# Kernel tuning notes

Measured on AMD Instinct MI355X. Metric: run time of the kernel, lower is better.

## Reference

```python
import jax, jax.numpy as jnp
import numpy as np

B, NPG, K = 8, 2048, 20   # graphs, nodes per graph, kNN fanout
N = B * NPG
OUT = 16


def _bn(h, g, b, eps=1e-5):
    # BatchNorm1d (training-mode batch stats, biased var), channels last
    ax = tuple(range(h.ndim - 1))
    m = h.mean(ax)
    v = h.var(ax)
    return g * (h - m) * jax.lax.rsqrt(v + eps) + b


def _mlp(h, w, b, g, be):
    # Sequential(Linear, ReLU, BatchNorm1d)
    return _bn(jax.nn.relu(h @ w + b), g, be)


def _knn(f, k):
    # k nearest (squared euclidean), self included like torch_cluster.knn(x, x)
    sq = jnp.sum(f * f, axis=-1)
    d = sq[:, None] - 2.0 * (f @ f.T) + sq[None, :]   # [n, n]
    return jax.lax.top_k(-d, k)[1]                    # [n, k]


def setup_inputs() -> dict:
    key = jax.random.key(0)
    ks = jax.random.split(key, 16)

    def w(i, shape):
        return jax.random.normal(ks[i], shape, jnp.float32) * (1.0 / np.sqrt(shape[0]))

    return {
        "pos": jax.random.normal(ks[0], (N, 3), jnp.float32),
        "x": jax.random.normal(ks[1], (N, 1), jnp.float32),
        "batch": jnp.repeat(jnp.arange(B, dtype=jnp.int32), NPG),  # equal-size graphs
        # conv1 edge MLP: Linear(8,64)+ReLU+BN
        "w1": w(2, (8, 64)), "b1": jnp.zeros((64,), jnp.float32), "g1": jnp.ones((64,), jnp.float32), "be1": jnp.zeros((64,), jnp.float32),
        # conv2 edge MLP: Linear(128,128)+ReLU+BN
        "w2": w(3, (128, 128)), "b2": jnp.zeros((128,), jnp.float32), "g2": jnp.ones((128,), jnp.float32), "be2": jnp.zeros((128,), jnp.float32),
        # fc: Linear(192,256)+ReLU+BN
        "wf": w(4, (192, 256)), "bf": jnp.zeros((256,), jnp.float32), "gf": jnp.ones((256,), jnp.float32), "bef": jnp.zeros((256,), jnp.float32),
        # out head: Linear(256,128)+ReLU+BN, Linear(128,64)+ReLU+BN, Linear(64,OUT)
        "wo1": w(5, (256, 128)), "bo1": jnp.zeros((128,), jnp.float32), "go1": jnp.ones((128,), jnp.float32), "beo1": jnp.zeros((128,), jnp.float32),
        "wo2": w(6, (128, 64)), "bo2": jnp.zeros((64,), jnp.float32), "go2": jnp.ones((64,), jnp.float32), "beo2": jnp.zeros((64,), jnp.float32),
        "wo3": w(7, (64, OUT)), "bo3": jnp.zeros((OUT,), jnp.float32),
    }


def reference(pos, x, batch, w1, b1, g1, be1, w2, b2, g2, be2,
              wf, bf, gf, bef, wo1, bo1, go1, beo1, wo2, bo2, go2, beo2, wo3, bo3):
    # ---- conv1: DynamicEdgeConv over ALL nodes (called without batch) ----
    f0 = jnp.concatenate([pos, x], axis=-1)            # [N, 4]
    idx1 = _knn(f0, K)                                 # [N, K] global kNN
    xi = f0[:, None, :]                                # [N, 1, 4]
    xj = jnp.take(f0, idx1, axis=0)                    # [N, K, 4]
    e1 = jnp.concatenate([jnp.broadcast_to(xi, xj.shape), xj - xi], axis=-1)  # [N,K,8]
    x1 = _mlp(e1, w1, b1, g1, be1).max(axis=1)         # max aggr -> [N, 64]

    # ---- conv2: DynamicEdgeConv with per-graph kNN (equal-size graphs) ----
    x1b = x1.reshape(B, NPG, -1)                       # [B, n, 64]
    idx2 = jax.vmap(lambda f: _knn(f, K))(x1b)         # [B, n, K] local indices
    xj2 = jax.vmap(lambda f, i: f[i])(x1b, idx2)       # [B, n, K, 64]
    xi2 = x1b[:, :, None, :]
    e2 = jnp.concatenate([jnp.broadcast_to(xi2, xj2.shape), xj2 - xi2], axis=-1)
    e2 = e2.reshape(N, K, 128)                         # BN over all edges jointly
    x2 = _mlp(e2, w2, b2, g2, be2).max(axis=1)         # [N, 128]

    # ---- fc + global max pool + head ----
    h = _mlp(jnp.concatenate([x1, x2], axis=-1), wf, bf, gf, bef)  # [N, 256]
    hp = h.reshape(B, NPG, -1).max(axis=1)             # global_max_pool -> [B, 256]
    hp = _mlp(hp, wo1, bo1, go1, beo1)                 # Dropout(0.5) = identity (eval)
    hp = _mlp(hp, wo2, bo2, go2, beo2)
    logits = hp @ wo3 + bo3                            # [B, OUT]
    return jax.nn.log_softmax(logits, axis=1)
```

## Files before the change

### kernel.cpp

```cpp
#include <hip/hip_runtime.h>
#include <math.h>

#define NPTS 16384
#define KNB 20
#define SCAP 512

typedef __attribute__((ext_vector_type(8))) short short8;
typedef __attribute__((ext_vector_type(4))) float f32x4;

static const size_t OFF_F0   = 0;
static const size_t OFF_SSQ0 = OFF_F0   + (size_t)NPTS*4*4;
static const size_t OFF_IDX1 = OFF_SSQ0 + (size_t)NPTS*4;
static const size_t OFF_XMX1 = OFF_IDX1 + (size_t)NPTS*KNB*4;
static const size_t OFF_XMN1 = OFF_XMX1 + (size_t)NPTS*64*4;
static const size_t OFF_SUM1 = OFF_XMN1 + (size_t)NPTS*64*4;
static const size_t OFF_X1   = OFF_SUM1 + 512;
static const size_t OFF_SSQ1 = OFF_X1   + (size_t)NPTS*64*4;
static const size_t OFF_IDX2 = OFF_SSQ1 + (size_t)NPTS*4;
static const size_t OFF_XMX2 = OFF_IDX2 + (size_t)NPTS*KNB*4;
static const size_t OFF_XMN2 = OFF_XMX2 + (size_t)NPTS*128*4;
static const size_t OFF_SUM2 = OFF_XMN2 + (size_t)NPTS*128*4;
static const size_t OFF_X2   = OFF_SUM2 + 1024;
static const size_t OFF_SUMF = OFF_X2   + (size_t)NPTS*128*4;
static const size_t OFF_HPMX = OFF_SUMF + 2048;
static const size_t OFF_HPMN = OFF_HPMX + 8*256*4;

__device__ __forceinline__ float dot4f(float4 a, float4 b) {
  return a.x*b.x + a.y*b.y + a.z*b.z + a.w*b.w;
}

__device__ __forceinline__ float dot64v(const float* a, const float4* b4) {
  float s = 0.f;
  #pragma unroll
  for (int d4 = 0; d4 < 16; ++d4) {
    float4 b = b4[d4];
    s += a[4*d4+0]*b.x + a[4*d4+1]*b.y + a[4*d4+2]*b.z + a[4*d4+3]*b.w;
  }
  return s;
}

__device__ __forceinline__ short f2bf(float x) {
  union { float f; unsigned u; } v; v.f = x;
  unsigned r = (v.u + 0x7FFFu + ((v.u >> 16) & 1u)) >> 16;
  return (short)r;
}

__device__ __forceinline__ void ce(float& a, int& ai, float& b, int& bi) {
  bool sw = b < a;
  float d0 = sw ? b : a;  float d1 = sw ? a : b;
  int   j0 = sw ? bi : ai; int  j1 = sw ? ai : bi;
  a = d0; ai = j0; b = d1; bi = j1;
}

__device__ __forceinline__ void sort16(float (&d)[16], int (&ix)[16]) {
  #pragma unroll
  for (int k = 2; k <= 16; k <<= 1) {
    #pragma unroll
    for (int j = k >> 1; j > 0; j >>= 1) {
      #pragma unroll
      for (int i = 0; i < 16; ++i) {
        int l = i ^ j;
        if (l > i) {
          if ((i & k) == 0) ce(d[i], ix[i], d[l], ix[l]);
          else              ce(d[l], ix[l], d[i], ix[i]);
        }
      }
    }
  }
}

__device__ __forceinline__ void bimerge32(float (&rd)[32], int (&ri)[32]) {
  #pragma unroll
  for (int j = 16; j > 0; j >>= 1) {
    #pragma unroll
    for (int i = 0; i < 32; ++i) {
      int l = i ^ j;
      if (l > i) ce(rd[i], ri[i], rd[l], ri[l]);
    }
  }
}

__device__ __forceinline__ void merge16(float (&rd)[32], int (&ri)[32],
                                        float (&bd)[16], int (&bi)[16]) {
  #pragma unroll
  for (int k = 0; k < 16; ++k) {
    bool sw = bd[15-k] < rd[16+k];
    rd[16+k] = sw ? bd[15-k] : rd[16+k];
    ri[16+k] = sw ? bi[15-k] : ri[16+k];
  }
  bimerge32(rd, ri);
}

__device__ __forceinline__ void mergelane(float (&rd)[32], int (&ri)[32], int mask) {
  float pd[32]; int pi[32];
  #pragma unroll
  for (int s = 0; s < 32; ++s) { pd[s] = __shfl_xor(rd[s], mask); pi[s] = __shfl_xor(ri[s], mask); }
  #pragma unroll
  for (int k = 0; k < 32; ++k) {
    bool sw = pd[31-k] < rd[k];
    rd[k] = sw ? pd[31-k] : rd[k];
    ri[k] = sw ? pi[31-k] : ri[k];
  }
  bimerge32(rd, ri);
}

__device__ __forceinline__ void vce(float& a, float& b) {
  float lo = fminf(a, b);
  b = fmaxf(a, b);
  a = lo;
}

__device__ __forceinline__ void vsort16(float (&d)[16]) {
  #pragma unroll
  for (int k = 2; k <= 16; k <<= 1) {
    #pragma unroll
    for (int j = k >> 1; j > 0; j >>= 1) {
      #pragma unroll
      for (int i = 0; i < 16; ++i) {
        int l = i ^ j;
        if (l > i) {
          if ((i & k) == 0) vce(d[i], d[l]);
          else              vce(d[l], d[i]);
        }
      }
    }
  }
}

__device__ __forceinline__ void vbimerge32(float (&rd)[32]) {
  #pragma unroll
  for (int j = 16; j > 0; j >>= 1) {
    #pragma unroll
    for (int i = 0; i < 32; ++i) {
      int l = i ^ j;
      if (l > i) vce(rd[i], rd[l]);
    }
  }
}

__device__ __forceinline__ void vmerge16(float (&rd)[32], float (&bd)[16]) {
  #pragma unroll
  for (int k = 0; k < 16; ++k) rd[16+k] = fminf(rd[16+k], bd[15-k]);
  vbimerge32(rd);
}

__device__ __forceinline__ void vmergelane(float (&rd)[32], int mask) {
  float pd[32];
  #pragma unroll
  for (int s = 0; s < 32; ++s) pd[s] = __shfl_xor(rd[s], mask);
  #pragma unroll
  for (int k = 0; k < 32; ++k) rd[k] = fminf(rd[k], pd[31-k]);
  vbimerge32(rd);
}

__global__ void k_init(float* sum1, float* sum2, float* sumF, unsigned* hpmx, unsigned* hpmn) {
  int t = blockIdx.x*256 + threadIdx.x;
  if (t < 128) sum1[t] = 0.f;
  if (t < 256) sum2[t] = 0.f;
  if (t < 512) sumF[t] = 0.f;
  if (t < 2048) { hpmx[t] = 0u; hpmn[t] = 0x7f800000u; }
}

__global__ __launch_bounds__(256) void k_f0(const float* __restrict__ pos, const float* __restrict__ x,
                                            float4* __restrict__ f0, float* __restrict__ ssq) {
  int i = blockIdx.x*256 + threadIdx.x;
  if (i >= NPTS) return;
  float4 f;
  f.x = pos[3*i+0]; f.y = pos[3*i+1]; f.z = pos[3*i+2]; f.w = x[i];
  f0[i] = f;
  ssq[i] = dot4f(f, f);
}

__global__ __launch_bounds__(256) void k_knn1(const float4* __restrict__ f0, const float* __restrict__ ssq,
                                              int* __restrict__ idx1) {
  __shared__ float2 surv[8][SCAP];
  __shared__ int scnt[8];
  __shared__ float rowT[8];
  int t = threadIdx.x;
  int r = t >> 5;
  int lane = t & 31;
  int row = blockIdx.x*8 + r;
  if (t < 8) scnt[t] = 0;
  float4 fi = f0[row];
  float sqi = ssq[row];
  {
    float rd[32];
    #pragma unroll
    for (int s = 0; s < 32; ++s) rd[s] = INFINITY;
    #pragma unroll
    for (int b = 0; b < 4; ++b) {
      float bd[16];
      #pragma unroll
      for (int u = 0; u < 16; ++u) {
        int j = b*512 + u*32 + lane;
        float4 c = f0[j];
        bd[u] = (sqi - 2.f*dot4f(fi, c)) + ssq[j];
      }
      vsort16(bd);
      vmerge16(rd, bd);
    }
    vmergelane(rd, 1); vmergelane(rd, 2); vmergelane(rd, 4);
    vmergelane(rd, 8); vmergelane(rd, 16);
    if (lane == 0) rowT[r] = rd[19];
  }
  __syncthreads();
  {
    float4 fr[8]; float sr[8], Tr[8];
    #pragma unroll
    for (int q = 0; q < 8; ++q) {
      fr[q] = f0[blockIdx.x*8 + q];
      sr[q] = ssq[blockIdx.x*8 + q];
      Tr[q] = rowT[q];
    }
    #pragma unroll 4
    for (int k = 0; k < 64; ++k) {
      int j = k*256 + t;
      float4 c = f0[j];
      float cq = ssq[j];
      #pragma unroll
      for (int q = 0; q < 8; ++q) {
        float d = (sr[q] - 2.f*dot4f(fr[q], c)) + cq;
        if (d <= Tr[q]) {
          int slot = atomicAdd(&scnt[q], 1);
          if (slot < SCAP) surv[q][slot] = make_float2(d, __int_as_float(j));
        }
      }
    }
  }
  __syncthreads();
  int n = scnt[r] < SCAP ? scnt[r] : SCAP;
  float rd[32]; int ri[32];
  #pragma unroll
  for (int s = 0; s < 32; ++s) { rd[s] = INFINITY; ri[s] = 0; }
  {
    float bd[16]; int bix[16];
    #pragma unroll
    for (int u = 0; u < 16; ++u) {
      int s = u*32 + lane;
      if (s < n) { float2 v = surv[r][s]; bd[u] = v.x; bix[u] = __float_as_int(v.y); }
      else       { bd[u] = INFINITY; bix[u] = 0; }
    }
    sort16(bd, bix);
    merge16(rd, ri, bd, bix);
  }
  mergelane(rd, ri, 1); mergelane(rd, ri, 2); mergelane(rd, ri, 4);
  mergelane(rd, ri, 8); mergelane(rd, ri, 16);
  if (lane == 0) {
    int4* p = (int4*)&idx1[row*KNB];
    p[0] = make_int4(ri[0],ri[1],ri[2],ri[3]);
    p[1] = make_int4(ri[4],ri[5],ri[6],ri[7]);
    p[2] = make_int4(ri[8],ri[9],ri[10],ri[11]);
    p[3] = make_int4(ri[12],ri[13],ri[14],ri[15]);
    p[4] = make_int4(ri[16],ri[17],ri[18],ri[19]);
  }
}

__global__ __launch_bounds__(256) void k_mlp1(const float4* __restrict__ f0, const int* __restrict__ idx1,
                                              const float* __restrict__ w1, const float* __restrict__ b1,
                                              float* __restrict__ xmx, float* __restrict__ xmn,
                                              float* __restrict__ sums) {
  __shared__ float rs[256], rs2[256];
  int t = threadIdx.x;
  int c = t & 63;
  int w = t >> 6;
  float wc[8];
  #pragma unroll
  for (int d = 0; d < 8; ++d) wc[d] = w1[d*64 + c];
  float bc = b1[c];
  float s = 0.f, s2 = 0.f;
  for (int p = 0; p < 8; ++p) {
    int i = blockIdx.x*32 + p*4 + w;
    float4 fi = f0[i];
    float mx = -INFINITY, mn = INFINITY;
    #pragma unroll
    for (int k = 0; k < KNB; ++k) {
      int j = idx1[i*KNB + k];
      float4 fj = f0[j];
      float h = bc + fi.x*wc[0] + fi.y*wc[1] + fi.z*wc[2] + fi.w*wc[3]
                   + (fj.x-fi.x)*wc[4] + (fj.y-fi.y)*wc[5] + (fj.z-fi.z)*wc[6] + (fj.w-fi.w)*wc[7];
      h = fmaxf(h, 0.f);
      mx = fmaxf(mx, h); mn = fminf(mn, h);
      s += h; s2 += h*h;
    }
    xmx[i*64+c] = mx; xmn[i*64+c] = mn;
  }
  rs[t] = s; rs2[t] = s2;
  __syncthreads();
  if (t < 64) {
    atomicAdd(&sums[c],      rs[t]+rs[t+64]+rs[t+128]+rs[t+192]);
    atomicAdd(&sums[64+c],   rs2[t]+rs2[t+64]+rs2[t+128]+rs2[t+192]);
  }
}

__global__ __launch_bounds__(256) void k_bn1apply(const float* __restrict__ sums, const float* __restrict__ g,
                                                  const float* __restrict__ be, const float* __restrict__ xmx,
                                                  const float* __restrict__ xmn, float* __restrict__ x1) {
  __shared__ float sc_s[64], sh_s[64];
  int t = threadIdx.x;
  if (t < 64) {
    float m = sums[t] * (1.f/327680.f);
    float v = sums[64+t] * (1.f/327680.f) - m*m;
    float sc = g[t] / sqrtf(v + 1e-5f);
    sc_s[t] = sc; sh_s[t] = be[t] - m*sc;
  }
  __syncthreads();
  int c = t & 63;
  int i = blockIdx.x*4 + (t>>6);
  float sc = sc_s[c], sh = sh_s[c];
  float val = (sc >= 0.f) ? xmx[i*64+c] : xmn[i*64+c];
  x1[i*64+c] = sc*val + sh;
}

__global__ __launch_bounds__(256) void k_wprep(const float* __restrict__ w2, short* __restrict__ wtg) {
  int t = blockIdx.x*256 + threadIdx.x;
  int c = t >> 7, k = t & 127;
  wtg[c*128 + k] = f2bf(w2[k*128 + c]);
}

__global__ __launch_bounds__(256) void k_ssq1(const float* __restrict__ x1, float* __restrict__ ssq1) {
  int i = blockIdx.x*256 + threadIdx.x;
  alignas(16) float f[64];
  #pragma unroll
  for (int d4 = 0; d4 < 16; ++d4) ((float4*)f)[d4] = ((const float4*)x1)[i*16 + d4];
  ssq1[i] = dot64v(f, (const float4*)f);
}

__global__ __launch_bounds__(256) void k_knn2(const float* __restrict__ x1, const float* __restrict__ ssq1,
                                              int* __restrict__ idx2) {
  __shared__ __align__(16) float tf[128][68];
  __shared__ float tq[128];
  int t = threadIdx.x;
  int row = blockIdx.x*32 + (t>>3);
  int lane = t & 7;
  int cbase = (row >> 11) << 11;
  alignas(16) float fi[64];
  #pragma unroll
  for (int d4 = 0; d4 < 16; ++d4) ((float4*)fi)[d4] = ((const float4*)x1)[row*16 + d4];
  float sqi = ssq1[row];
  float rd[32]; int ri[32];
  #pragma unroll
  for (int s = 0; s < 32; ++s) { rd[s] = INFINITY; ri[s] = 0; }
  for (int tile = 0; tile < 16; ++tile) {
    int base = cbase + tile*128;
    __syncthreads();
    for (int v = t; v < 128*16; v += 256) {
      int jl = v >> 4, d4 = v & 15;
      *(float4*)&tf[jl][d4*4] = ((const float4*)x1)[(base+jl)*16 + d4];
    }
    if (t < 128) tq[t] = ssq1[base + t];
    __syncthreads();
    float bd[16]; int bix[16];
    #pragma unroll
    for (int u = 0; u < 16; ++u) {
      int jl = u*8 + lane;
      bd[u] = (sqi - 2.f*dot64v(fi, (const float4*)&tf[jl][0])) + tq[jl];
      bix[u] = base + jl;
    }
    sort16(bd, bix);
    merge16(rd, ri, bd, bix);
  }
  mergelane(rd, ri, 1);
  mergelane(rd, ri, 2);
  mergelane(rd, ri, 4);
  if (lane == 0) {
    int4* p = (int4*)&idx2[row*KNB];
    p[0] = make_int4(ri[0],ri[1],ri[2],ri[3]);
    p[1] = make_int4(ri[4],ri[5],ri[6],ri[7]);
    p[2] = make_int4(ri[8],ri[9],ri[10],ri[11]);
    p[3] = make_int4(ri[12],ri[13],ri[14],ri[15]);
    p[4] = make_int4(ri[16],ri[17],ri[18],ri[19]);
  }
}

__global__ __launch_bounds__(256) void k_mlp2(const float* __restrict__ x1, const int* __restrict__ idx2,
                                              const short* __restrict__ wtg, const float* __restrict__ b2,
                                              float* __restrict__ xmx, float* __restrict__ xmn,
                                              float* __restrict__ sums) {
  __shared__ __align__(16) short Elds[4*32*136];
  __shared__ int js[4][KNB];
  int t = threadIdx.x;
  if (t < 4*KNB) js[t/KNB][t%KNB] = idx2[blockIdx.x*4*KNB + t];
  __syncthreads();
  #pragma unroll
  for (int cc = 0; cc < 8; ++cc) {
    int v = t + cc*256;
    int p  = v >> 9;
    int rr = (v >> 4) & 31;
    int kc = v & 15;
    short8 outv = {0,0,0,0,0,0,0,0};
    if (rr < KNB) {
      int i = blockIdx.x*4 + p;
      float4 a0, a1;
      if (kc < 8) {
        a0 = ((const float4*)x1)[i*16 + kc*2];
        a1 = ((const float4*)x1)[i*16 + kc*2 + 1];
      } else {
        int j = js[p][rr];
        int kk = kc - 8;
        float4 j0 = ((const float4*)x1)[j*16 + kk*2];
        float4 j1 = ((const float4*)x1)[j*16 + kk*2 + 1];
        float4 i0 = ((const float4*)x1)[i*16 + kk*2];
        float4 i1 = ((const float4*)x1)[i*16 + kk*2 + 1];
        a0 = make_float4(j0.x-i0.x, j0.y-i0.y, j0.z-i0.z, j0.w-i0.w);
        a1 = make_float4(j1.x-i1.x, j1.y-i1.y, j1.z-i1.z, j1.w-i1.w);
      }
      outv[0]=f2bf(a0.x); outv[1]=f2bf(a0.y); outv[2]=f2bf(a0.z); outv[3]=f2bf(a0.w);
      outv[4]=f2bf(a1.x); outv[5]=f2bf(a1.y); outv[6]=f2bf(a1.z); outv[7]=f2bf(a1.w);
    }
    *(short8*)&Elds[p*4352 + rr*136 + kc*8] = outv;
  }
  __syncthreads();
  int w = t >> 6, l = t & 63;
  int colA = w*32 + (l & 15);
  int colB = colA + 16;
  short8 bf[2][4];
  #pragma unroll
  for (int n = 0; n < 2; ++n)
    #pragma unroll
    for (int kb = 0; kb < 4; ++kb) {
      int col = w*32 + n*16 + (l & 15);
      int k0 = kb*32 + (l >> 4)*8;
      bf[n][kb] = *(const short8*)&wtg[col*128 + k0];
    }
  float bc0 = b2[colA], bc1 = b2[colB];
  float sT0=0.f, qT0=0.f, sT1=0.f, qT1=0.f;
  #pragma unroll
  for (int p = 0; p < 4; ++p) {
    int i = blockIdx.x*4 + p;
    float mx0=-INFINITY, mn0=INFINITY, s0=0.f, q0=0.f;
    float mx1=-INFINITY, mn1=INFINITY, s1=0.f, q1=0.f;
    #pragma unroll
    for (int m = 0; m < 2; ++m) {
      short8 af[4];
      #pragma unroll
      for (int kb = 0; kb < 4; ++kb) {
        int row = m*16 + (l & 15);
        int k0 = kb*32 + (l >> 4)*8;
        af[kb] = *(short8*)&Elds[p*4352 + row*136 + k0];
      }
      f32x4 acc0 = {0.f,0.f,0.f,0.f};
      f32x4 acc1 = {0.f,0.f,0.f,0.f};
      #pragma unroll
      for (int kb = 0; kb < 4; ++kb) {
        acc0 = __builtin_amdgcn_mfma_f32_16x16x32_bf16(af[kb], bf[0][kb], acc0, 0, 0, 0);
        acc1 = __builtin_amdgcn_mfma_f32_16x16x32_bf16(af[kb], bf[1][kb], acc1, 0, 0, 0);
      }
      int rbase = (l >> 4)*4 + m*16;
      #pragma unroll
      for (int reg = 0; reg < 4; ++reg) {
        bool valid = (rbase + reg) < KNB;
        float h0 = fmaxf(acc0[reg] + bc0, 0.f);
        float h1 = fmaxf(acc1[reg] + bc1, 0.f);
        if (valid) {
          mx0 = fmaxf(mx0, h0); mn0 = fminf(mn0, h0); s0 += h0; q0 += h0*h0;
          mx1 = fmaxf(mx1, h1); mn1 = fminf(mn1, h1); s1 += h1; q1 += h1*h1;
        }
      }
    }
    #pragma unroll
    for (int dlt = 16; dlt <= 32; dlt <<= 1) {
      mx0 = fmaxf(mx0, __shfl_xor(mx0, dlt)); mn0 = fminf(mn0, __shfl_xor(mn0, dlt));
      s0 += __shfl_xor(s0, dlt);              q0 += __shfl_xor(q0, dlt);
      mx1 = fmaxf(mx1, __shfl_xor(mx1, dlt)); mn1 = fminf(mn1, __shfl_xor(mn1, dlt));
      s1 += __shfl_xor(s1, dlt);              q1 += __shfl_xor(q1, dlt);
    }
    if (l < 16) {
      xmx[i*128 + colA] = mx0; xmx[i*128 + colB] = mx1;
      xmn[i*128 + colA] = mn0; xmn[i*128 + colB] = mn1;
    }
    sT0 += s0; qT0 += q0; sT1 += s1; qT1 += q1;
  }
  if (l < 16) {
    atomicAdd(&sums[colA], sT0);       atomicAdd(&sums[colB], sT1);
    atomicAdd(&sums[128 + colA], qT0); atomicAdd(&sums[128 + colB], qT1);
  }
}

__global__ __launch_bounds__(256) void k_bn2apply(const float* __restrict__ sums, const float* __restrict__ g,
                                                  const float* __restrict__ be, const float* __restrict__ xmx,
                                                  const float* __restrict__ xmn, float* __restrict__ x2) {
  __shared__ float sc_s[128], sh_s[128];
  int t = threadIdx.x;
  if (t < 128) {
    float m = sums[t] * (1.f/327680.f);
    float v = sums[128+t] * (1.f/327680.f) - m*m;
    float sc = g[t] / sqrtf(v + 1e-5f);
    sc_s[t] = sc; sh_s[t] = be[t] - m*sc;
  }
  __syncthreads();
  int c = t & 127;
  int i = blockIdx.x*2 + (t>>7);
  float sc = sc_s[c], sh = sh_s[c];
  float val = (sc >= 0.f) ? xmx[i*128+c] : xmn[i*128+c];
  x2[i*128+c] = sc*val + sh;
}

__global__ __launch_bounds__(256) void k_gemmF(const float* __restrict__ x1, const float* __restrict__ x2,
                                               const float* __restrict__ wf, const float* __restrict__ bf,
                                               float* __restrict__ sumsF, unsigned* __restrict__ hpmx,
                                               unsigned* __restrict__ hpmn) {
  __shared__ float A_s[64*193];
  __shared__ __align__(16) float B_s[192*64];
  __shared__ float red[1024];
  int t = threadIdx.x;
  int rt = blockIdx.x >> 2;
  int ct = blockIdx.x & 3;
  for (int v = t; v < 64*48; v += 256) {
    int r = v / 48, gg = v - r*48;
    int row = rt*64 + r;
    float4 e = (gg < 16) ? ((const float4*)x1)[row*16 + gg]
                         : ((const float4*)x2)[row*32 + (gg-16)];
    float* p = &A_s[r*193 + gg*4];
    p[0]=e.x; p[1]=e.y; p[2]=e.z; p[3]=e.w;
  }
  for (int v = t; v < 192*16; v += 256) {
    int d = v >> 4, c4 = v & 15;
    *(float4*)&B_s[d*64 + c4*4] = ((const float4*)wf)[d*64 + ct*16 + c4];
  }
  __syncthreads();
  int rg = t & 15, cg = t >> 4;
  float acc[4][4];
  #pragma unroll
  for (int a=0;a<4;a++) { acc[a][0]=0.f; acc[a][1]=0.f; acc[a][2]=0.f; acc[a][3]=0.f; }
  for (int d = 0; d < 192; ++d) {
    float a0 = A_s[(rg*4+0)*193 + d];
    float a1 = A_s[(rg*4+1)*193 + d];
    float a2 = A_s[(rg*4+2)*193 + d];
    float a3 = A_s[(rg*4+3)*193 + d];
    float b0 = B_s[d*64 + cg];
    float b1 = B_s[d*64 + cg + 16];
    float b2 = B_s[d*64 + cg + 32];
    float b3 = B_s[d*64 + cg + 48];
    acc[0][0]+=a0*b0; acc[0][1]+=a0*b1; acc[0][2]+=a0*b2; acc[0][3]+=a0*b3;
    acc[1][0]+=a1*b0; acc[1][1]+=a1*b1; acc[1][2]+=a1*b2; acc[1][3]+=a1*b3;
    acc[2][0]+=a2*b0; acc[2][1]+=a2*b1; acc[2][2]+=a2*b2; acc[2][3]+=a2*b3;
    acc[3][0]+=a3*b0; acc[3][1]+=a3*b1; acc[3][2]+=a3*b2; acc[3][3]+=a3*b3;
  }
  float hv[4][4];
  #pragma unroll
  for (int ss=0; ss<4; ++ss) {
    float bb = bf[ct*64 + cg + ss*16];
    #pragma unroll
    for (int rr=0; rr<4; ++rr) hv[rr][ss] = fmaxf(acc[rr][ss] + bb, 0.f);
  }
  int b = rt >> 5;
  #pragma unroll
  for (int ss=0; ss<4; ++ss) red[rg*64 + cg + ss*16] = hv[0][ss]+hv[1][ss]+hv[2][ss]+hv[3][ss];
  __syncthreads();
  if (t < 64) {
    float v = 0.f;
    #pragma unroll
    for (int r=0;r<16;r++) v += red[r*64 + t];
    atomicAdd(&sumsF[ct*64 + t], v);
  }
  __syncthreads();
  #pragma unroll
  for (int ss=0; ss<4; ++ss) red[rg*64 + cg + ss*16] =
      hv[0][ss]*hv[0][ss]+hv[1][ss]*hv[1][ss]+hv[2][ss]*hv[2][ss]+hv[3][ss]*hv[3][ss];
  __syncthreads();
  if (t < 64) {
    float v = 0.f;
    #pragma unroll
    for (int r=0;r<16;r++) v += red[r*64 + t];
    atomicAdd(&sumsF[256 + ct*64 + t], v);
  }
  __syncthreads();
  #pragma unroll
  for (int ss=0; ss<4; ++ss) red[rg*64 + cg + ss*16] =
      fmaxf(fmaxf(hv[0][ss],hv[1][ss]), fmaxf(hv[2][ss],hv[3][ss]));
  __syncthreads();
  if (t < 64) {
    float v = -INFINITY;
    #pragma unroll
    for (int r=0;r<16;r++) v = fmaxf(v, red[r*64 + t]);
    atomicMax(&hpmx[b*256 + ct*64 + t], __float_as_uint(v));
  }
  __syncthreads();
  #pragma unroll
  for (int ss=0; ss<4; ++ss) red[rg*64 + cg + ss*16] =
      fminf(fminf(hv[0][ss],hv[1][ss]), fminf(hv[2][ss],hv[3][ss]));
  __syncthreads();
  if (t < 64) {
    float v = INFINITY;
    #pragma unroll
    for (int r=0;r<16;r++) v = fminf(v, red[r*64 + t]);
    atomicMin(&hpmn[b*256 + ct*64 + t], __float_as_uint(v));
  }
}

__global__ __launch_bounds__(256) void k_head(const float* __restrict__ sumsF, const float* __restrict__ gf,
                                              const float* __restrict__ bef,
                                              const unsigned* __restrict__ hpmx, const unsigned* __restrict__ hpmn,
                                              const float* __restrict__ wo1, const float* __restrict__ bo1,
                                              const float* __restrict__ go1, const float* __restrict__ beo1,
                                              const float* __restrict__ wo2, const float* __restrict__ bo2,
                                              const float* __restrict__ go2, const float* __restrict__ beo2,
                                              const float* __restrict__ wo3, const float* __restrict__ bo3,
                                              float* __restrict__ out) {
  __shared__ float hp[8][256];
  __shared__ float u1[8][128];
  __shared__ float u2[8][64];
  __shared__ float lg[8][16];
  int t = threadIdx.x;
  {
    float m = sumsF[t] * (1.f/16384.f);
    float v = sumsF[256+t] * (1.f/16384.f) - m*m;
    float sc = gf[t] / sqrtf(v + 1e-5f);
    float sh = bef[t] - m*sc;
    for (int b = 0; b < 8; ++b) {
      unsigned bits = (sc >= 0.f) ? hpmx[b*256+t] : hpmn[b*256+t];
      hp[b][t] = sc*__uint_as_float(bits) + sh;
    }
  }
  __syncthreads();
  for (int p = t; p < 1024; p += 256) {
    int b = p >> 7, c = p & 127;
    float z = bo1[c];
    for (int d = 0; d < 256; ++d) z += hp[b][d]*wo1[d*128+c];
    u1[b][c] = fmaxf(z, 0.f);
  }
  __syncthreads();
  if (t < 128) {
    float m = 0.f;
    for (int b=0;b<8;b++) m += u1[b][t];
    m *= 0.125f;
    float v = 0.f;
    for (int b=0;b<8;b++) { float dd = u1[b][t]-m; v += dd*dd; }
    v *= 0.125f;
    float sc = go1[t]/sqrtf(v+1e-5f), sh = beo1[t]-m*sc;
    for (int b=0;b<8;b++) u1[b][t] = sc*u1[b][t]+sh;
  }
  __syncthreads();
  for (int p = t; p < 512; p += 256) {
    int b = p >> 6, c = p & 63;
    float z = bo2[c];
    for (int d = 0; d < 128; ++d) z += u1[b][d]*wo2[d*64+c];
    u2[b][c] = fmaxf(z, 0.f);
  }
  __syncthreads();
  if (t < 64) {
    float m = 0.f;
    for (int b=0;b<8;b++) m += u2[b][t];
    m *= 0.125f;
    float v = 0.f;
    for (int b=0;b<8;b++) { float dd = u2[b][t]-m; v += dd*dd; }
    v *= 0.125f;
    float sc = go2[t]/sqrtf(v+1e-5f), sh = beo2[t]-m*sc;
    for (int b=0;b<8;b++) u2[b][t] = sc*u2[b][t]+sh;
  }
  __syncthreads();
  if (t < 128) {
    int b = t >> 4, c = t & 15;
    float z = bo3[c];
    for (int d = 0; d < 64; ++d) z += u2[b][d]*wo3[d*16+c];
    lg[b][c] = z;
  }
  __syncthreads();
  if (t < 8) {
    float m = -INFINITY;
    for (int j=0;j<16;j++) m = fmaxf(m, lg[t][j]);
    float s = 0.f;
    for (int j=0;j<16;j++) s += expf(lg[t][j]-m);
    float ls = logf(s);
    for (int j=0;j<16;j++) out[t*16+j] = (lg[t][j]-m) - ls;
  }
}

extern "C" void kernel_launch(void* const* d_in, const int* in_sizes, int n_in,
                              void* d_out, int out_size, void* d_ws, size_t ws_size,
                              hipStream_t stream) {
  (void)in_sizes; (void)n_in; (void)out_size; (void)ws_size;
  const float* pos = (const float*)d_in[0];
  const float* x   = (const float*)d_in[1];
  const float* w1  = (const float*)d_in[3];
  const float* b1  = (const float*)d_in[4];
  const float* g1  = (const float*)d_in[5];
  const float* be1 = (const float*)d_in[6];
  const float* w2  = (const float*)d_in[7];
  const float* b2  = (const float*)d_in[8];
  const float* g2  = (const float*)d_in[9];
  const float* be2 = (const float*)d_in[10];
  const float* wf  = (const float*)d_in[11];
  const float* bf  = (const float*)d_in[12];
  const float* gf  = (const float*)d_in[13];
  const float* bef = (const float*)d_in[14];
  const float* wo1 = (const float*)d_in[15];
  const float* bo1 = (const float*)d_in[16];
  const float* go1 = (const float*)d_in[17];
  const float* beo1= (const float*)d_in[18];
  const float* wo2 = (const float*)d_in[19];
  const float* bo2 = (const float*)d_in[20];
  const float* go2 = (const float*)d_in[21];
  const float* beo2= (const float*)d_in[22];
  const float* wo3 = (const float*)d_in[23];
  const float* bo3 = (const float*)d_in[24];

  char* ws = (char*)d_ws;
  float4*   f0    = (float4*)  (ws + OFF_F0);
  float*    ssq0  = (float*)   (ws + OFF_SSQ0);
  int*      idx1  = (int*)     (ws + OFF_IDX1);
  float*    xmx1  = (float*)   (ws + OFF_XMX1);
  float*    xmn1  = (float*)   (ws + OFF_XMN1);
  float*    sum1  = (float*)   (ws + OFF_SUM1);
  float*    x1    = (float*)   (ws + OFF_X1);
  float*    ssq1  = (float*)   (ws + OFF_SSQ1);
  int*      idx2  = (int*)     (ws + OFF_IDX2);
  float*    xmx2  = (float*)   (ws + OFF_XMX2);
  float*    xmn2  = (float*)   (ws + OFF_XMN2);
  float*    sum2  = (float*)   (ws + OFF_SUM2);
  float*    x2    = (float*)   (ws + OFF_X2);
  float*    sumF  = (float*)   (ws + OFF_SUMF);
  unsigned* hpmx  = (unsigned*)(ws + OFF_HPMX);
  unsigned* hpmn  = (unsigned*)(ws + OFF_HPMN);
  short*    wtg   = (short*)   (ws + OFF_XMX1);

  k_init    <<<8,    256, 0, stream>>>(sum1, sum2, sumF, hpmx, hpmn);
  k_f0      <<<64,   256, 0, stream>>>(pos, x, f0, ssq0);
  k_knn1    <<<2048, 256, 0, stream>>>(f0, ssq0, idx1);
  k_mlp1    <<<512,  256, 0, stream>>>(f0, idx1, w1, b1, xmx1, xmn1, sum1);
  k_bn1apply<<<4096, 256, 0, stream>>>(sum1, g1, be1, xmx1, xmn1, x1);
  k_wprep   <<<64,   256, 0, stream>>>(w2, wtg);
  k_ssq1    <<<64,   256, 0, stream>>>(x1, ssq1);
  k_knn2    <<<512,  256, 0, stream>>>(x1, ssq1, idx2);
  k_mlp2    <<<4096, 256, 0, stream>>>(x1, idx2, wtg, b2, xmx2, xmn2, sum2);
  k_bn2apply<<<8192, 256, 0, stream>>>(sum2, g2, be2, xmx2, xmn2, x2);
  k_gemmF   <<<1024, 256, 0, stream>>>(x1, x2, wf, bf, sumF, hpmx, hpmn);
  k_head    <<<1,    256, 0, stream>>>(sumF, gf, bef, hpmx, hpmn,
                                       wo1, bo1, go1, beo1, wo2, bo2, go2, beo2, wo3, bo3,
                                       (float*)d_out);
}
```

Baseline: 682.8 us.

## Split conv2 edge GEMM into per-point xi term and neighbour-diff MFMA

Rewrites the conv2 edge Linear as W_top·xi + W_bot·(xj−xi). The xi term is computed once per point in fp32 and seeded into the MFMA accumulators, so the MFMA K dimension and the LDS edge tile are halved. The init, feature-prep and weight-transpose kernels are merged into one launch, and the transposed weights are moved to the x2 workspace slot. The exchange is a scalar per-point 64-term dot product per column in each block, with w2 read from global memory.

Measured after the change: 671.0 us. No clear change (-1.7%).

```diff
diff --git a/kernel.cpp b/kernel.cpp
--- a/kernel.cpp
+++ b/kernel.cpp
@@ -153,22 +153,22 @@
   vbimerge32(rd);
 }
 
-__global__ void k_init(float* sum1, float* sum2, float* sumF, unsigned* hpmx, unsigned* hpmn) {
-  int t = blockIdx.x*256 + threadIdx.x;
-  if (t < 128) sum1[t] = 0.f;
-  if (t < 256) sum2[t] = 0.f;
-  if (t < 512) sumF[t] = 0.f;
-  if (t < 2048) { hpmx[t] = 0u; hpmn[t] = 0x7f800000u; }
-}
-
-__global__ __launch_bounds__(256) void k_f0(const float* __restrict__ pos, const float* __restrict__ x,
-                                            float4* __restrict__ f0, float* __restrict__ ssq) {
-  int i = blockIdx.x*256 + threadIdx.x;
-  if (i >= NPTS) return;
+__global__ __launch_bounds__(256) void k_init(const float* __restrict__ pos, const float* __restrict__ x,
+                                              const float* __restrict__ w2,
+                                              float4* __restrict__ f0, float* __restrict__ ssq,
+                                              short* __restrict__ wtg,
+                                              float* sum1, float* sum2, float* sumF,
+                                              unsigned* hpmx, unsigned* hpmn) {
+  int gt = blockIdx.x*256 + threadIdx.x;
   float4 f;
-  f.x = pos[3*i+0]; f.y = pos[3*i+1]; f.z = pos[3*i+2]; f.w = x[i];
-  f0[i] = f;
-  ssq[i] = dot4f(f, f);
+  f.x = pos[3*gt+0]; f.y = pos[3*gt+1]; f.z = pos[3*gt+2]; f.w = x[gt];
+  f0[gt] = f;
+  ssq[gt] = dot4f(f, f);
+  { int c = gt >> 7, k = gt & 127; wtg[c*128 + k] = f2bf(w2[k*128 + c]); }
+  if (gt < 128) sum1[gt] = 0.f;
+  if (gt < 256) sum2[gt] = 0.f;
+  if (gt < 512) sumF[gt] = 0.f;
+  if (gt < 2048) { hpmx[gt] = 0u; hpmn[gt] = 0x7f800000u; }
 }
 
 __global__ __launch_bounds__(256) void k_knn1(const float4* __restrict__ f0, const float* __restrict__ ssq,
@@ -311,12 +311,6 @@
   x1[i*64+c] = sc*val + sh;
 }
 
-__global__ __launch_bounds__(256) void k_wprep(const float* __restrict__ w2, short* __restrict__ wtg) {
-  int t = blockIdx.x*256 + threadIdx.x;
-  int c = t >> 7, k = t & 127;
-  wtg[c*128 + k] = f2bf(w2[k*128 + c]);
-}
-
 __global__ __launch_bounds__(256) void k_ssq1(const float* __restrict__ x1, float* __restrict__ ssq1) {
   int i = blockIdx.x*256 + threadIdx.x;
   alignas(16) float f[64];
@@ -373,84 +367,89 @@
 }
 
 __global__ __launch_bounds__(256) void k_mlp2(const float* __restrict__ x1, const int* __restrict__ idx2,
-                                              const short* __restrict__ wtg, const float* __restrict__ b2,
+                                              const short* __restrict__ wtg, const float* __restrict__ w2,
+                                              const float* __restrict__ b2,
                                               float* __restrict__ xmx, float* __restrict__ xmn,
                                               float* __restrict__ sums) {
-  __shared__ __align__(16) short Elds[4*32*136];
+  __shared__ __align__(16) short Elds[4*32*72];
+  __shared__ float xi_s[4][64];
+  __shared__ float vi[4][128];
   __shared__ int js[4][KNB];
   int t = threadIdx.x;
   if (t < 4*KNB) js[t/KNB][t%KNB] = idx2[blockIdx.x*4*KNB + t];
-  __syncthreads();
-  #pragma unroll
-  for (int cc = 0; cc < 8; ++cc) {
+  {
+    int p = t >> 6, k = t & 63;
+    xi_s[p][k] = x1[(blockIdx.x*4 + p)*64 + k];
+  }
+  __syncthreads();
+  #pragma unroll
+  for (int v2 = 0; v2 < 2; ++v2) {
+    int v = t + v2*256;
+    int p = v >> 7, c = v & 127;
+    float a = b2[c];
+    #pragma unroll 8
+    for (int k = 0; k < 64; ++k) a += xi_s[p][k] * w2[k*128 + c];
+    vi[p][c] = a;
+  }
+  #pragma unroll
+  for (int cc = 0; cc < 4; ++cc) {
     int v = t + cc*256;
-    int p  = v >> 9;
-    int rr = (v >> 4) & 31;
-    int kc = v & 15;
+    int p  = v >> 8;
+    int rr = (v >> 3) & 31;
+    int kc = v & 7;
     short8 outv = {0,0,0,0,0,0,0,0};
     if (rr < KNB) {
-      int i = blockIdx.x*4 + p;
-      float4 a0, a1;
-      if (kc < 8) {
-        a0 = ((const float4*)x1)[i*16 + kc*2];
-        a1 = ((const float4*)x1)[i*16 + kc*2 + 1];
-      } else {
-        int j = js[p][rr];
-        int kk = kc - 8;
-        float4 j0 = ((const float4*)x1)[j*16 + kk*2];
-        float4 j1 = ((const float4*)x1)[j*16 + kk*2 + 1];
-        float4 i0 = ((const float4*)x1)[i*16 + kk*2];
-        float4 i1 = ((const float4*)x1)[i*16 + kk*2 + 1];
-        a0 = make_float4(j0.x-i0.x, j0.y-i0.y, j0.z-i0.z, j0.w-i0.w);
-        a1 = make_float4(j1.x-i1.x, j1.y-i1.y, j1.z-i1.z, j1.w-i1.w);
-      }
-      outv[0]=f2bf(a0.x); outv[1]=f2bf(a0.y); outv[2]=f2bf(a0.z); outv[3]=f2bf(a0.w);
-      outv[4]=f2bf(a1.x); outv[5]=f2bf(a1.y); outv[6]=f2bf(a1.z); outv[7]=f2bf(a1.w);
-    }
-    *(short8*)&Elds[p*4352 + rr*136 + kc*8] = outv;
+      int j = js[p][rr];
+      float4 j0 = ((const float4*)x1)[j*16 + kc*2];
+      float4 j1 = ((const float4*)x1)[j*16 + kc*2 + 1];
+      const float* xp = &xi_s[p][kc*8];
+      outv[0]=f2bf(j0.x-xp[0]); outv[1]=f2bf(j0.y-xp[1]); outv[2]=f2bf(j0.z-xp[2]); outv[3]=f2bf(j0.w-xp[3]);
+      outv[4]=f2bf(j1.x-xp[4]); outv[5]=f2bf(j1.y-xp[5]); outv[6]=f2bf(j1.z-xp[6]); outv[7]=f2bf(j1.w-xp[7]);
+    }
+    *(short8*)&Elds[p*2304 + rr*72 + kc*8] = outv;
   }
   __syncthreads();
   int w = t >> 6, l = t & 63;
   int colA = w*32 + (l & 15);
   int colB = colA + 16;
-  short8 bf[2][4];
+  short8 bfr[2][2];
   #pragma unroll
   for (int n = 0; n < 2; ++n)
     #pragma unroll
-    for (int kb = 0; kb < 4; ++kb) {
+    for (int kb = 0; kb < 2; ++kb) {
       int col = w*32 + n*16 + (l & 15);
-      int k0 = kb*32 + (l >> 4)*8;
-      bf[n][kb] = *(const short8*)&wtg[col*128 + k0];
-    }
-  float bc0 = b2[colA], bc1 = b2[colB];
+      int k0 = 64 + kb*32 + (l >> 4)*8;
+      bfr[n][kb] = *(const short8*)&wtg[col*128 + k0];
+    }
   float sT0=0.f, qT0=0.f, sT1=0.f, qT1=0.f;
   #pragma unroll
   for (int p = 0; p < 4; ++p) {
     int i = blockIdx.x*4 + p;
+    float vA = vi[p][colA], vB = vi[p][colB];
     float mx0=-INFINITY, mn0=INFINITY, s0=0.f, q0=0.f;
     float mx1=-INFINITY, mn1=INFINITY, s1=0.f, q1=0.f;
     #pragma unroll
     for (int m = 0; m < 2; ++m) {
-      short8 af[4];
+      short8 af[2];
       #pragma unroll
-      for (int kb = 0; kb < 4; ++kb) {
+      for (int kb = 0; kb < 2; ++kb) {
         int row = m*16 + (l & 15);
         int k0 = kb*32 + (l >> 4)*8;
-        af[kb] = *(short8*)&Elds[p*4352 + row*136 + k0];
+        af[kb] = *(short8*)&Elds[p*2304 + row*72 + k0];
       }
-      f32x4 acc0 = {0.f,0.f,0.f,0.f};
-      f32x4 acc1 = {0.f,0.f,0.f,0.f};
+      f32x4 acc0 = {vA, vA, vA, vA};
+      f32x4 acc1 = {vB, vB, vB, vB};
       #pragma unroll
-      for (int kb = 0; kb < 4; ++kb) {
-        acc0 = __builtin_amdgcn_mfma_f32_16x16x32_bf16(af[kb], bf[0][kb], acc0, 0, 0, 0);
-        acc1 = __builtin_amdgcn_mfma_f32_16x16x32_bf16(af[kb], bf[1][kb], acc1, 0, 0, 0);
+      for (int kb = 0; kb < 2; ++kb) {
+        acc0 = __builtin_amdgcn_mfma_f32_16x16x32_bf16(af[kb], bfr[0][kb], acc0, 0, 0, 0);
+        acc1 = __builtin_amdgcn_mfma_f32_16x16x32_bf16(af[kb], bfr[1][kb], acc1, 0, 0, 0);
       }
       int rbase = (l >> 4)*4 + m*16;
       #pragma unroll
       for (int reg = 0; reg < 4; ++reg) {
         bool valid = (rbase + reg) < KNB;
-        float h0 = fmaxf(acc0[reg] + bc0, 0.f);
-        float h1 = fmaxf(acc1[reg] + bc1, 0.f);
+        float h0 = fmaxf(acc0[reg], 0.f);
+        float h1 = fmaxf(acc1[reg], 0.f);
         if (valid) {
           mx0 = fmaxf(mx0, h0); mn0 = fminf(mn0, h0); s0 += h0; q0 += h0*h0;
           mx1 = fmaxf(mx1, h1); mn1 = fminf(mn1, h1); s1 += h1; q1 += h1*h1;
@@ -712,17 +711,15 @@
   float*    sumF  = (float*)   (ws + OFF_SUMF);
   unsigned* hpmx  = (unsigned*)(ws + OFF_HPMX);
   unsigned* hpmn  = (unsigned*)(ws + OFF_HPMN);
-  short*    wtg   = (short*)   (ws + OFF_XMX1);
-
-  k_init    <<<8,    256, 0, stream>>>(sum1, sum2, sumF, hpmx, hpmn);
-  k_f0      <<<64,   256, 0, stream>>>(pos, x, f0, ssq0);
+  short*    wtg   = (short*)   (ws + OFF_X2);
+
+  k_init    <<<64,   256, 0, stream>>>(pos, x, w2, f0, ssq0, wtg, sum1, sum2, sumF, hpmx, hpmn);
   k_knn1    <<<2048, 256, 0, stream>>>(f0, ssq0, idx1);
   k_mlp1    <<<512,  256, 0, stream>>>(f0, idx1, w1, b1, xmx1, xmn1, sum1);
   k_bn1apply<<<4096, 256, 0, stream>>>(sum1, g1, be1, xmx1, xmn1, x1);
-  k_wprep   <<<64,   256, 0, stream>>>(w2, wtg);
   k_ssq1    <<<64,   256, 0, stream>>>(x1, ssq1);
   k_knn2    <<<512,  256, 0, stream>>>(x1, ssq1, idx2);
-  k_mlp2    <<<4096, 256, 0, stream>>>(x1, idx2, wtg, b2, xmx2, xmn2, sum2);
+  k_mlp2    <<<4096, 256, 0, stream>>>(x1, idx2, wtg, w2, b2, xmx2, xmn2, sum2);
   k_bn2apply<<<8192, 256, 0, stream>>>(sum2, g2, be2, xmx2, xmn2, x2);
   k_gemmF   <<<1024, 256, 0, stream>>>(x1, x2, wf, bf, sumF, hpmx, hpmn);
   k_head    <<<1,    256, 0, stream>>>(sumF, gf, bef, hpmx, hpmn,
```
